# Optimization experiments

Measured on AMD Instinct MI355X. Metric: run time of the kernel, lower is better.

## Reference

```python
import jax, jax.numpy as jnp
import numpy as np

M_SAMPLES = 256
IN_DIM = 512          # original in_dim (before +1 bias row)
R = IN_DIM + 1        # 513
C = 512               # out_dim


def setup_inputs() -> dict:
    key = jax.random.key(0)
    k1, k2, k3, k4 = jax.random.split(key, 4)
    x = jax.random.normal(k1, (M_SAMPLES, IN_DIM), dtype=jnp.float32)
    mu = jax.random.normal(k2, (C, R), dtype=jnp.float32)
    var = jax.random.uniform(k3, (C, R), dtype=jnp.float32)  # positive diagonal variances
    E = jax.random.normal(k4, (M_SAMPLES, C, R), dtype=jnp.float32)  # per-sample epsilon
    return {"x": x, "mu": mu, "var": var, "E": E, "shape": IN_DIM}


def reference(x, mu, var, E, shape):
    m = x.shape[0]
    x = x.reshape(m, shape)
    # append bias column of ones -> [m, r]
    x = jnp.concatenate([x, jnp.ones((m, 1), dtype=x.dtype)], axis=1)
    # diagonal covariance: per-sample weight W = mu + sqrt(var) * eps, shape [m, c, r]
    W = mu + jnp.sqrt(var) * E
    # bmm(x[m,1,r], W.transpose(1,2)[m,r,c]).squeeze(1) == einsum over r
    h = jnp.einsum('mr,mcr->mc', x, W)  # [m, c]
    return h
```

## Files before the change

### kernel.cpp

```cpp
#include <hip/hip_runtime.h>
#include <math.h>
#include <stdint.h>

#define Rdim 513
#define SM_ELEMS (512 * Rdim)

typedef float v4f  __attribute__((ext_vector_type(4)));
typedef uint32_t v4u __attribute__((ext_vector_type(4)));

__device__ __forceinline__ uint32_t rne_bf16(float x) {
    uint32_t u = __float_as_uint(x);
    return (u + 0x7FFFu + ((u >> 16) & 1u)) >> 16;
}

__global__ __launch_bounds__(256) void pack_sm_kernel(const float* __restrict__ var,
                                                      const float* __restrict__ mu,
                                                      uint32_t* __restrict__ sm, int n) {
    int i = blockIdx.x * 256 + threadIdx.x;
    if (i < n) {
        uint32_t sb = rne_bf16(sqrtf(var[i]));
        uint32_t mb = rne_bf16(mu[i]);
        sm[i] = (mb << 16) | sb;
    }
}

__device__ __forceinline__ float bf_mu(uint32_t u) { return __uint_as_float(u & 0xFFFF0000u); }
__device__ __forceinline__ float bf_sg(uint32_t u) { return __uint_as_float(u << 16); }

__global__ __launch_bounds__(256) void bnn_kernel(const float* __restrict__ x,
                                                  const uint32_t* __restrict__ SM,
                                                  const float* __restrict__ E,
                                                  float* __restrict__ out) {
    const int lane = threadIdx.x & 63;
    const int wid  = threadIdx.x >> 6;
    const int row  = blockIdx.x * 4 + wid;
    const int m    = row >> 9;
    const int c    = row & 511;

    const int q    = c & 3;
    const int pad  = (4 - q) & 3;
    const int CH   = pad ? 127 : 128;
    const int eA   = pad + 4 * lane;
    const int eB   = pad + 4 * (CH - 64 + lane);

    const size_t eb = (size_t)row * (size_t)Rdim;
    const size_t cb = (size_t)c   * (size_t)Rdim;
    const float* __restrict__ xr = x + m * 512;

    float xA0 = xr[eA], xA1 = xr[eA + 1], xA2 = xr[eA + 2], xA3 = xr[eA + 3];
    float xB0 = xr[eB], xB1 = xr[eB + 1], xB2 = xr[eB + 2], xB3 = xr[eB + 3];
    if (pad && lane == 0) { xB0 = xB1 = xB2 = xB3 = 0.f; }

    const int nS = pad ? 5 : 1;
    int se = -1;
    if (lane < nS) se = (lane < pad) ? lane : (pad + 4 * CH + (lane - pad));
    const float xs = (se >= 0) ? ((se < 512) ? xr[se] : 1.0f) : 0.0f;

    const v4f Ea = *(const v4f*)(E  + eb + eA);
    const v4f Eb = *(const v4f*)(E  + eb + eB);
    const v4u Pa = *(const v4u*)(SM + cb + eA);
    const v4u Pb = *(const v4u*)(SM + cb + eB);
    float Es = 0.f, xs_mu = 0.f, xs_sg = 0.f;
    if (se >= 0) {
        Es = E[eb + se];
        uint32_t Ps = SM[cb + se];
        xs_mu = bf_mu(Ps); xs_sg = bf_sg(Ps);
    }

    float acc;
    acc =            xA0 * fmaf(bf_sg(Pa.x), Ea.x, bf_mu(Pa.x));
    acc = fmaf(xA1, fmaf(bf_sg(Pa.y), Ea.y, bf_mu(Pa.y)), acc);
    acc = fmaf(xA2, fmaf(bf_sg(Pa.z), Ea.z, bf_mu(Pa.z)), acc);
    acc = fmaf(xA3, fmaf(bf_sg(Pa.w), Ea.w, bf_mu(Pa.w)), acc);
    acc = fmaf(xB0, fmaf(bf_sg(Pb.x), Eb.x, bf_mu(Pb.x)), acc);
    acc = fmaf(xB1, fmaf(bf_sg(Pb.y), Eb.y, bf_mu(Pb.y)), acc);
    acc = fmaf(xB2, fmaf(bf_sg(Pb.z), Eb.z, bf_mu(Pb.z)), acc);
    acc = fmaf(xB3, fmaf(bf_sg(Pb.w), Eb.w, bf_mu(Pb.w)), acc);
    acc = fmaf(xs,  fmaf(xs_sg, Es, xs_mu), acc);

#pragma unroll
    for (int off = 32; off >= 1; off >>= 1)
        acc += __shfl_xor(acc, off, 64);

    if (lane == 0) out[row] = acc;
}

extern "C" void kernel_launch(void* const* d_in, const int* in_sizes, int n_in,
                              void* d_out, int out_size, void* d_ws, size_t ws_size,
                              hipStream_t stream) {
    const float* x   = (const float*)d_in[0];
    const float* mu  = (const float*)d_in[1];
    const float* var = (const float*)d_in[2];
    const float* E   = (const float*)d_in[3];
    float* out = (float*)d_out;

    uint32_t* SM = (uint32_t*)d_ws;
    pack_sm_kernel<<<(SM_ELEMS + 255) / 256, 256, 0, stream>>>(var, mu, SM, SM_ELEMS);
    bnn_kernel<<<32768, 256, 0, stream>>>(x, SM, E, out);
}
```

Baseline: 51.97 us.

## Process two samples per wavefront to reuse packed mu/sigma loads

Each wavefront now computes outputs for two consecutive samples sharing the same output column, so the packed bf16 mu/sigma row is loaded once and applied to both samples' epsilon rows. The two accumulators are merged through a lane-parity swap shuffle followed by a shared butterfly reduction, which saves one shuffle chain. The grid is halved. The kernel is dominated by streaming E, so the gain is limited to fewer SM loads and less per-wave overhead, at the cost of more registers and fewer waves in flight.

```diff
diff --git a/kernel.cpp b/kernel.cpp
--- a/kernel.cpp
+++ b/kernel.cpp
@@ -32,10 +32,12 @@
                                                   const float* __restrict__ E,
                                                   float* __restrict__ out) {
     const int lane = threadIdx.x & 63;
-    const int wid  = threadIdx.x >> 6;
-    const int row  = blockIdx.x * 4 + wid;
-    const int m    = row >> 9;
-    const int c    = row & 511;
+    const int w    = threadIdx.x >> 6;
+    const int b    = blockIdx.x;
+    const int mg   = b >> 7;
+    const int cg   = b & 127;
+    const int c    = cg * 4 + w;
+    const int m0   = mg * 2;
 
     const int q    = c & 3;
     const int pad  = (4 - q) & 3;
@@ -43,46 +45,69 @@
     const int eA   = pad + 4 * lane;
     const int eB   = pad + 4 * (CH - 64 + lane);
 
-    const size_t eb = (size_t)row * (size_t)Rdim;
-    const size_t cb = (size_t)c   * (size_t)Rdim;
-    const float* __restrict__ xr = x + m * 512;
+    const size_t row0 = (size_t)m0 * 512 + c;
+    const size_t eb0  = row0 * (size_t)Rdim;
+    const size_t eb1  = eb0 + (size_t)512 * Rdim;
+    const size_t cb   = (size_t)c * (size_t)Rdim;
+    const float* __restrict__ xr0 = x + m0 * 512;
+    const float* __restrict__ xr1 = xr0 + 512;
 
-    float xA0 = xr[eA], xA1 = xr[eA + 1], xA2 = xr[eA + 2], xA3 = xr[eA + 3];
-    float xB0 = xr[eB], xB1 = xr[eB + 1], xB2 = xr[eB + 2], xB3 = xr[eB + 3];
-    if (pad && lane == 0) { xB0 = xB1 = xB2 = xB3 = 0.f; }
+    const v4u Pa  = *(const v4u*)(SM + cb + eA);
+    const v4u Pb  = *(const v4u*)(SM + cb + eB);
+    const v4f E0a = *(const v4f*)(E + eb0 + eA);
+    const v4f E0b = *(const v4f*)(E + eb0 + eB);
+    const v4f E1a = *(const v4f*)(E + eb1 + eA);
+    const v4f E1b = *(const v4f*)(E + eb1 + eB);
+
+    float x0A0 = xr0[eA], x0A1 = xr0[eA+1], x0A2 = xr0[eA+2], x0A3 = xr0[eA+3];
+    float x0B0 = xr0[eB], x0B1 = xr0[eB+1], x0B2 = xr0[eB+2], x0B3 = xr0[eB+3];
+    float x1A0 = xr1[eA], x1A1 = xr1[eA+1], x1A2 = xr1[eA+2], x1A3 = xr1[eA+3];
+    float x1B0 = xr1[eB], x1B1 = xr1[eB+1], x1B2 = xr1[eB+2], x1B3 = xr1[eB+3];
+    if (pad && lane == 0) {
+        x0B0 = x0B1 = x0B2 = x0B3 = 0.f;
+        x1B0 = x1B1 = x1B2 = x1B3 = 0.f;
+    }
 
     const int nS = pad ? 5 : 1;
     int se = -1;
     if (lane < nS) se = (lane < pad) ? lane : (pad + 4 * CH + (lane - pad));
-    const float xs = (se >= 0) ? ((se < 512) ? xr[se] : 1.0f) : 0.0f;
-
-    const v4f Ea = *(const v4f*)(E  + eb + eA);
-    const v4f Eb = *(const v4f*)(E  + eb + eB);
-    const v4u Pa = *(const v4u*)(SM + cb + eA);
-    const v4u Pb = *(const v4u*)(SM + cb + eB);
-    float Es = 0.f, xs_mu = 0.f, xs_sg = 0.f;
+    float xs0 = 0.f, xs1 = 0.f, Es0 = 0.f, Es1 = 0.f, ls_mu = 0.f, ls_sg = 0.f;
     if (se >= 0) {
-        Es = E[eb + se];
+        xs0 = (se < 512) ? xr0[se] : 1.0f;
+        xs1 = (se < 512) ? xr1[se] : 1.0f;
+        Es0 = E[eb0 + se];
+        Es1 = E[eb1 + se];
         uint32_t Ps = SM[cb + se];
-        xs_mu = bf_mu(Ps); xs_sg = bf_sg(Ps);
+        ls_mu = bf_mu(Ps); ls_sg = bf_sg(Ps);
     }
 
-    float acc;
-    acc =            xA0 * fmaf(bf_sg(Pa.x), Ea.x, bf_mu(Pa.x));
-    acc = fmaf(xA1, fmaf(bf_sg(Pa.y), Ea.y, bf_mu(Pa.y)), acc);
-    acc = fmaf(xA2, fmaf(bf_sg(Pa.z), Ea.z, bf_mu(Pa.z)), acc);
-    acc = fmaf(xA3, fmaf(bf_sg(Pa.w), Ea.w, bf_mu(Pa.w)), acc);
-    acc = fmaf(xB0, fmaf(bf_sg(Pb.x), Eb.x, bf_mu(Pb.x)), acc);
-    acc = fmaf(xB1, fmaf(bf_sg(Pb.y), Eb.y, bf_mu(Pb.y)), acc);
-    acc = fmaf(xB2, fmaf(bf_sg(Pb.z), Eb.z, bf_mu(Pb.z)), acc);
-    acc = fmaf(xB3, fmaf(bf_sg(Pb.w), Eb.w, bf_mu(Pb.w)), acc);
-    acc = fmaf(xs,  fmaf(xs_sg, Es, xs_mu), acc);
+    float sgx, mux, acc0, acc1;
+#define TERM(P, Ev0, Ev1, X0, X1)                                   \
+    sgx = bf_sg(P); mux = bf_mu(P);                                 \
+    acc0 = fmaf(X0, fmaf(sgx, Ev0, mux), acc0);                     \
+    acc1 = fmaf(X1, fmaf(sgx, Ev1, mux), acc1);
 
+    acc0 = 0.f; acc1 = 0.f;
+    TERM(Pa.x, E0a.x, E1a.x, x0A0, x1A0)
+    TERM(Pa.y, E0a.y, E1a.y, x0A1, x1A1)
+    TERM(Pa.z, E0a.z, E1a.z, x0A2, x1A2)
+    TERM(Pa.w, E0a.w, E1a.w, x0A3, x1A3)
+    TERM(Pb.x, E0b.x, E1b.x, x0B0, x1B0)
+    TERM(Pb.y, E0b.y, E1b.y, x0B1, x1B1)
+    TERM(Pb.z, E0b.z, E1b.z, x0B2, x1B2)
+    TERM(Pb.w, E0b.w, E1b.w, x0B3, x1B3)
+    acc0 = fmaf(xs0, fmaf(ls_sg, Es0, ls_mu), acc0);
+    acc1 = fmaf(xs1, fmaf(ls_sg, Es1, ls_mu), acc1);
+#undef TERM
+
+    float keep = (lane & 1) ? acc1 : acc0;
+    float send = (lane & 1) ? acc0 : acc1;
+    float v = keep + __shfl_xor(send, 1, 64);
 #pragma unroll
-    for (int off = 32; off >= 1; off >>= 1)
-        acc += __shfl_xor(acc, off, 64);
+    for (int off = 2; off <= 32; off <<= 1)
+        v += __shfl_xor(v, off, 64);
 
-    if (lane == 0) out[row] = acc;
+    if (lane < 2) out[row0 + (size_t)lane * 512] = v;
 }
 
 extern "C" void kernel_launch(void* const* d_in, const int* in_sizes, int n_in,
@@ -96,5 +121,5 @@
 
     uint32_t* SM = (uint32_t*)d_ws;
     pack_sm_kernel<<<(SM_ELEMS + 255) / 256, 256, 0, stream>>>(var, mu, SM, SM_ELEMS);
-    bnn_kernel<<<32768, 256, 0, stream>>>(x, SM, E, out);
+    bnn_kernel<<<16384, 256, 0, stream>>>(x, SM, E, out);
 }
```

After: 51.08 us. No clear change (-1.7%).
